# Kernel optimization log

Measured on AMD Instinct MI355X. Metric: run time of the kernel, lower is better.

Reference implementation:

```python
import jax, jax.numpy as jnp
import numpy as np

N = 50000   # nodes
E = 800000  # edges (before self loops)
IN_DIM = 64
HID = 128
HEADS = 4
DH = HID // HEADS  # 32 per-head out_feats
L = 3
EPS = 1e-5
NEG_SLOPE = 0.2


def setup_inputs() -> dict:
    key = jax.random.key(0)
    ks = jax.random.split(key, 10)
    s = 0.1  # weight scale for numerical sanity
    return {
        "node_feats": jax.random.normal(ks[0], (N, IN_DIM), jnp.float32),
        "src": jax.random.randint(ks[1], (E,), 0, N, dtype=jnp.int32),
        "dst": jax.random.randint(ks[2], (E,), 0, N, dtype=jnp.int32),
        "W_in": jax.random.normal(ks[3], (IN_DIM, HID), jnp.float32) * s,
        "b_in": jnp.zeros((HID,), jnp.float32),
        "W_src": jax.random.normal(ks[4], (L, HID, HID), jnp.float32) * s,
        "b_src": jnp.zeros((L, HID), jnp.float32),
        "W_dst": jax.random.normal(ks[5], (L, HID, HID), jnp.float32) * s,
        "b_dst": jnp.zeros((L, HID), jnp.float32),
        "attn": jax.random.normal(ks[6], (L, HEADS, DH), jnp.float32) * s,
        "ln_g": jnp.ones((L, HID), jnp.float32),
        "ln_b": jnp.zeros((L, HID), jnp.float32),
    }


def _layer_norm(x, g, b):
    mu = jnp.mean(x, axis=-1, keepdims=True)
    var = jnp.mean((x - mu) ** 2, axis=-1, keepdims=True)
    return (x - mu) * jax.lax.rsqrt(var + EPS) * g + b


def _gatv2(h, s_idx, d_idx, Ws, bs, Wd, bd, a):
    # h: [N, HID]; edges s_idx -> d_idx (self loops included)
    fs = (h @ Ws + bs).reshape(N, HEADS, DH)  # W_src h, source features
    fd = (h @ Wd + bd).reshape(N, HEADS, DH)  # W_dst h, dest features
    e = jax.nn.leaky_relu(fs[s_idx] + fd[d_idx], NEG_SLOPE)   # [E', H, D]
    logits = jnp.einsum('ehd,hd->eh', e, a)                   # [E', H]
    # segment softmax over incoming edges of each destination node
    m = jax.ops.segment_max(logits, d_idx, num_segments=N)    # [N, H]
    p = jnp.exp(logits - m[d_idx])
    z = jax.ops.segment_sum(p, d_idx, num_segments=N)         # [N, H]
    alpha = p / z[d_idx]                                      # [E', H]
    msg = fs[s_idx] * alpha[..., None]                        # [E', H, D]
    out = jax.ops.segment_sum(msg, d_idx, num_segments=N)     # [N, H, D]
    out = out + h.reshape(N, HEADS, DH)  # residual (Identity res_fc)
    return out.reshape(N, HID)


def reference(node_feats, src, dst, W_in, b_in, W_src, b_src, W_dst, b_dst, attn, ln_g, ln_b):
    loop = jnp.arange(N, dtype=src.dtype)
    s_idx = jnp.concatenate([src, loop])  # add_self_loop
    d_idx = jnp.concatenate([dst, loop])
    h = node_feats @ W_in + b_in
    for l in range(L):
        h_new = _gatv2(h, s_idx, d_idx, W_src[l], b_src[l], W_dst[l], b_dst[l], attn[l])
        h = _layer_norm(h + h_new, ln_g[l], ln_b[l])
        h = jax.nn.relu(h)
    graph_emb = jnp.mean(h, axis=0, keepdims=True)  # dgl.mean_nodes, batch of 1 graph
    return graph_emb, h
```

## Files before the change

kernel.cpp:

```cpp
#include <hip/hip_runtime.h>
#include <hip/hip_bf16.h>

#define NN 50000
#define CSTRIDE 16

typedef short short8 __attribute__((ext_vector_type(8)));
typedef float f32x4 __attribute__((ext_vector_type(4)));

#define GLOBAL_AS __attribute__((address_space(1)))
#define LDS_AS __attribute__((address_space(3)))

__device__ __forceinline__ unsigned short f2bf(float f) {
    unsigned int b = __float_as_uint(f);
    unsigned int r = (b + 0x7FFFu + ((b >> 16) & 1u)) >> 16;
    return (unsigned short)r;
}
__device__ __forceinline__ float bf2f(unsigned short u) {
    return __uint_as_float((unsigned int)u << 16);
}


__global__ __launch_bounds__(256, 4) void prep_kernel(
        const int* __restrict__ dst, int* countsS, int* __restrict__ rank, int E,
        const float* __restrict__ Ws, const float* __restrict__ Wd,
        unsigned short* __restrict__ WtL,
        const float* __restrict__ x, const float* __restrict__ Win,
        const float* __restrict__ bin, unsigned short* __restrict__ hB) {
    int HB = (E + 255) >> 8;
    int blk = blockIdx.x;
    if (blk < HB) {
        int i = blk * 256 + threadIdx.x;
        if (i < E) rank[i] = atomicAdd(&countsS[(size_t)dst[i] * CSTRIDE], 1);
        return;
    }
    if (blk < HB + 384) {
        int e = (blk - HB) * 256 + threadIdx.x;
        int l = e >> 15;
        int r = e & 32767;
        int colc = r >> 7;
        int k = r & 127;
        float v = (colc < 128) ? Ws[l * 16384 + k * 128 + colc]
                               : Wd[l * 16384 + k * 128 + (colc - 128)];
        WtL[l * 32768 + colc * 128 + k] = f2bf(v);
        return;
    }
    int blk0 = blk - HB - 384;
    int tid = threadIdx.x;
    int w = tid >> 6, l = tid & 63;
    int m = l & 15, q = l >> 4;
    short8 B[2][2];
    #pragma unroll
    for (int ct = 0; ct < 2; ++ct) {
        int colw = w * 32 + ct * 16 + m;
        #pragma unroll
        for (int kt = 0; kt < 2; ++kt) {
            short8 a;
            #pragma unroll
            for (int jj = 0; jj < 8; ++jj)
                a[jj] = (short)f2bf(Win[(kt * 32 + q * 8 + jj) * 128 + colw]);
            B[ct][kt] = a;
        }
    }
    float bias[2];
    #pragma unroll
    for (int ct = 0; ct < 2; ++ct) bias[ct] = bin[w * 32 + ct * 16 + m];
    for (int rg = blk0; rg < NN / 16; rg += 512) {
        int row0 = rg * 16;
        const float* ap = x + (size_t)(row0 + m) * 64 + q * 8;
        short8 A[2];
        #pragma unroll
        for (int kt = 0; kt < 2; ++kt) {
            float4 f0 = *(const float4*)(ap + kt * 32);
            float4 f1 = *(const float4*)(ap + kt * 32 + 4);
            short8 a;
            a[0] = (short)f2bf(f0.x); a[1] = (short)f2bf(f0.y);
            a[2] = (short)f2bf(f0.z); a[3] = (short)f2bf(f0.w);
            a[4] = (short)f2bf(f1.x); a[5] = (short)f2bf(f1.y);
            a[6] = (short)f2bf(f1.z); a[7] = (short)f2bf(f1.w);
            A[kt] = a;
        }
        f32x4 acc[2];
        #pragma unroll
        for (int ct = 0; ct < 2; ++ct) acc[ct] = (f32x4){0.f, 0.f, 0.f, 0.f};
        #pragma unroll
        for (int kt = 0; kt < 2; ++kt)
            #pragma unroll
            for (int ct = 0; ct < 2; ++ct)
                acc[ct] = __builtin_amdgcn_mfma_f32_16x16x32_bf16(A[kt], B[ct][kt], acc[ct], 0, 0, 0);
        #pragma unroll
        for (int ct = 0; ct < 2; ++ct) {
            int colw = w * 32 + ct * 16 + m;
            #pragma unroll
            for (int i = 0; i < 4; ++i) {
                int row = row0 + q * 4 + i;
                hB[(size_t)row * 128 + colw] = f2bf(acc[ct][i] + bias[ct]);
            }
        }
    }
}

__global__ __launch_bounds__(256) void alloc_kernel(const int* __restrict__ countsS,
                                                    int* __restrict__ row_beg,
                                                    int* total, int n) {
    int i = blockIdx.x * blockDim.x + threadIdx.x;
    int lane = threadIdx.x & 63;
    int len = (i < n) ? (countsS[(size_t)i * CSTRIDE] + 1) : 0;
    int p = len;
    #pragma unroll
    for (int off = 1; off < 64; off <<= 1) {
        int t = __shfl_up(p, off);
        if (lane >= off) p += t;
    }
    int tot = __shfl(p, 63);
    int base = 0;
    if (lane == 63) base = atomicAdd(total, tot);
    base = __shfl(base, 63);
    if (i < n) row_beg[i] = base + p - len;
}

__device__ __forceinline__ void dual_body(const unsigned short* __restrict__ hB,
                                          const unsigned short* __restrict__ Wt,
                                          const float* __restrict__ bs,
                                          const float* __restrict__ bd,
                                          unsigned short* __restrict__ fsB,
                                          unsigned short* __restrict__ fdB,
                                          unsigned short* Atile, int t0, int tstride) {
    int tid = threadIdx.x;
    int w = tid >> 6, l = tid & 63;
    int m = l & 15, q = l >> 4;
    short8 B[4][4];
    #pragma unroll
    for (int ct = 0; ct < 4; ++ct) {
        int colw = w * 64 + ct * 16 + m;
        const unsigned short* wp = Wt + colw * 128 + q * 8;
        #pragma unroll
        for (int kt = 0; kt < 4; ++kt) B[ct][kt] = *(const short8*)(wp + kt * 32);
    }
    const float* bptr = (w < 2) ? bs : bd;
    unsigned short* OUT = (w < 2) ? fsB : fdB;
    int ocb = (w * 64) & 127;
    float bias[4];
    #pragma unroll
    for (int ct = 0; ct < 4; ++ct) bias[ct] = bptr[ocb + ct * 16 + m];

    const int NT = (NN + 63) / 64;
    for (int t = t0; t < NT; t += tstride) {
        int row0 = t * 64;
        const char* gsrc = (const char*)(hB + (size_t)row0 * 128);
        #pragma unroll
        for (int c = 0; c < 4; ++c) {
            int off = c * 4096 + tid * 16;
            __builtin_amdgcn_global_load_lds((const GLOBAL_AS void*)(gsrc + off),
                                             (LDS_AS void*)((char*)Atile + off), 16, 0, 0);
        }
        __syncthreads();
        #pragma unroll
        for (int rg = 0; rg < 4; ++rg) {
            const unsigned short* ap = Atile + (rg * 16 + m) * 128 + q * 8;
            short8 A[4];
            #pragma unroll
            for (int kt = 0; kt < 4; ++kt) A[kt] = *(const short8*)(ap + kt * 32);
            f32x4 acc[4];
            #pragma unroll
            for (int ct = 0; ct < 4; ++ct) acc[ct] = (f32x4){0.f, 0.f, 0.f, 0.f};
            #pragma unroll
            for (int kt = 0; kt < 4; ++kt)
                #pragma unroll
                for (int ct = 0; ct < 4; ++ct)
                    acc[ct] = __builtin_amdgcn_mfma_f32_16x16x32_bf16(A[kt], B[ct][kt], acc[ct], 0, 0, 0);
            #pragma unroll
            for (int ct = 0; ct < 4; ++ct) {
                int colw = ocb + ct * 16 + m;
                #pragma unroll
                for (int i = 0; i < 4; ++i) {
                    int row = row0 + rg * 16 + q * 4 + i;
                    if (row < NN) OUT[(size_t)row * 128 + colw] = f2bf(acc[ct][i] + bias[ct]);
                }
            }
        }
        __syncthreads();
    }
}

__global__ __launch_bounds__(256, 4) void scatter_dual_kernel(
        const int* __restrict__ src, const int* __restrict__ dst,
        const int* __restrict__ rank, const int* __restrict__ row_beg,
        const int* __restrict__ countsS, int* __restrict__ col, int E, int n,
        const unsigned short* __restrict__ hB, const unsigned short* __restrict__ Wt,
        const float* __restrict__ bs, const float* __restrict__ bd,
        unsigned short* __restrict__ fsB, unsigned short* __restrict__ fdB) {
    __shared__ unsigned short Atile[64 * 128];
    int SB = (E + n + 255) >> 8;
    if ((int)blockIdx.x < SB) {
        int i = blockIdx.x * 256 + threadIdx.x;
        if (i >= E + n) return;
        if (i < E) {
            col[row_beg[dst[i]] + rank[i]] = src[i];
        } else {
            int v = i - E;
            col[row_beg[v] + countsS[(size_t)v * CSTRIDE]] = v;
        }
        return;
    }
    dual_body(hB, Wt, bs, bd, fsB, fdB, Atile, blockIdx.x - SB, gridDim.x - SB);
}

__global__ __launch_bounds__(256, 4) void dual_gemm_mfma(const unsigned short* __restrict__ hB,
                                                         const unsigned short* __restrict__ Wt,
                                                         const float* __restrict__ bs,
                                                         const float* __restrict__ bd,
                                                         unsigned short* __restrict__ fsB,
                                                         unsigned short* __restrict__ fdB) {
    __shared__ unsigned short Atile[64 * 128];
    dual_body(hB, Wt, bs, bd, fsB, fdB, Atile, blockIdx.x, gridDim.x);
}

__global__ __launch_bounds__(256) void agg_ln_kernel(const unsigned short* __restrict__ h_in,
                                                     const unsigned short* __restrict__ fsB,
                                                     const unsigned short* __restrict__ fdB,
                                                     const int* __restrict__ row_beg,
                                                     const int* __restrict__ countsS,
                                                     const int* __restrict__ col,
                                                     const float* __restrict__ attn,
                                                     const float* __restrict__ ln_g,
                                                     const float* __restrict__ ln_b,
                                                     unsigned short* __restrict__ hb_out,
                                                     float* __restrict__ hf_out, int n) {
    int gwave = (blockIdx.x * blockDim.x + threadIdx.x) >> 6;
    int lane = threadIdx.x & 63;
    int half = lane >> 5;
    int sub = lane & 31;
    int node = gwave * 2 + half;
    if (node >= n) return;
    int f0 = 4 * sub;
    unsigned foff = (unsigned)(f0 * 2);
    const char* fsp = (const char*)fsB;
    ushort4 ud = *(const ushort4*)((const char*)fdB + (((unsigned)node << 8) | foff));
    float4 fd4;
    fd4.x = bf2f(ud.x); fd4.y = bf2f(ud.y); fd4.z = bf2f(ud.z); fd4.w = bf2f(ud.w);
    ushort4 uh = *(const ushort4*)((const char*)h_in + (((unsigned)node << 8) | foff));
    float4 h4;
    h4.x = bf2f(uh.x); h4.y = bf2f(uh.y); h4.z = bf2f(uh.z); h4.w = bf2f(uh.w);
    const float4 a4 = *(const float4*)(attn + f0);
    float4 a06, a04;
    a06.x = 0.6f * a4.x; a06.y = 0.6f * a4.y; a06.z = 0.6f * a4.z; a06.w = 0.6f * a4.w;
    a04.x = 0.4f * a4.x; a04.y = 0.4f * a4.y; a04.z = 0.4f * a4.z; a04.w = 0.4f * a4.w;
    int beg = row_beg[node], end = beg + countsS[(size_t)node * CSTRIDE] + 1;

    float z[4];
    float4 acc[4];
    #pragma unroll
    for (int k = 0; k < 4; ++k) {
        z[k] = 0.f;
        acc[k].x = 0.f; acc[k].y = 0.f; acc[k].z = 0.f; acc[k].w = 0.f;
    }

    int j = beg;
    for (; j + 3 < end; j += 4) {
        int s0 = col[j], s1 = col[j + 1], s2 = col[j + 2], s3 = col[j + 3];
        ushort4 u0 = *(const ushort4*)(fsp + (((unsigned)s0 << 8) | foff));
        ushort4 u1 = *(const ushort4*)(fsp + (((unsigned)s1 << 8) | foff));
        ushort4 u2 = *(const ushort4*)(fsp + (((unsigned)s2 << 8) | foff));
        ushort4 u3 = *(const ushort4*)(fsp + (((unsigned)s3 << 8) | foff));
        float4 v0, v1, v2, v3;
        v0.x = bf2f(u0.x); v0.y = bf2f(u0.y); v0.z = bf2f(u0.z); v0.w = bf2f(u0.w);
        v1.x = bf2f(u1.x); v1.y = bf2f(u1.y); v1.z = bf2f(u1.z); v1.w = bf2f(u1.w);
        v2.x = bf2f(u2.x); v2.y = bf2f(u2.y); v2.z = bf2f(u2.z); v2.w = bf2f(u2.w);
        v3.x = bf2f(u3.x); v3.y = bf2f(u3.y); v3.z = bf2f(u3.z); v3.w = bf2f(u3.w);
        float p0, p1, p2, p3;
        {
            float e0 = v0.x + fd4.x, e1 = v0.y + fd4.y, e2 = v0.z + fd4.z, e3 = v0.w + fd4.w;
            p0 = e0 * a06.x + fabsf(e0) * a04.x + e1 * a06.y + fabsf(e1) * a04.y
               + e2 * a06.z + fabsf(e2) * a04.z + e3 * a06.w + fabsf(e3) * a04.w;
        }
        {
            float e0 = v1.x + fd4.x, e1 = v1.y + fd4.y, e2 = v1.z + fd4.z, e3 = v1.w + fd4.w;
            p1 = e0 * a06.x + fabsf(e0) * a04.x + e1 * a06.y + fabsf(e1) * a04.y
               + e2 * a06.z + fabsf(e2) * a04.z + e3 * a06.w + fabsf(e3) * a04.w;
        }
        {
            float e0 = v2.x + fd4.x, e1 = v2.y + fd4.y, e2 = v2.z + fd4.z, e3 = v2.w + fd4.w;
            p2 = e0 * a06.x + fabsf(e0) * a04.x + e1 * a06.y + fabsf(e1) * a04.y
               + e2 * a06.z + fabsf(e2) * a04.z + e3 * a06.w + fabsf(e3) * a04.w;
        }
        {
            float e0 = v3.x + fd4.x, e1 = v3.y + fd4.y, e2 = v3.z + fd4.z, e3 = v3.w + fd4.w;
            p3 = e0 * a06.x + fabsf(e0) * a04.x + e1 * a06.y + fabsf(e1) * a04.y
               + e2 * a06.z + fabsf(e2) * a04.z + e3 * a06.w + fabsf(e3) * a04.w;
        }
        #pragma unroll
        for (int off = 1; off <= 4; off <<= 1) {
            p0 += __shfl_xor(p0, off);
            p1 += __shfl_xor(p1, off);
            p2 += __shfl_xor(p2, off);
            p3 += __shfl_xor(p3, off);
        }
        float w0 = __expf(p0), w1 = __expf(p1), w2 = __expf(p2), w3 = __expf(p3);
        z[0] += w0; z[1] += w1; z[2] += w2; z[3] += w3;
        acc[0].x += w0 * v0.x; acc[0].y += w0 * v0.y; acc[0].z += w0 * v0.z; acc[0].w += w0 * v0.w;
        acc[1].x += w1 * v1.x; acc[1].y += w1 * v1.y; acc[1].z += w1 * v1.z; acc[1].w += w1 * v1.w;
        acc[2].x += w2 * v2.x; acc[2].y += w2 * v2.y; acc[2].z += w2 * v2.z; acc[2].w += w2 * v2.w;
        acc[3].x += w3 * v3.x; acc[3].y += w3 * v3.y; acc[3].z += w3 * v3.z; acc[3].w += w3 * v3.w;
    }
    for (; j < end; ++j) {
        int s = col[j];
        ushort4 u = *(const ushort4*)(fsp + (((unsigned)s << 8) | foff));
        float4 v;
        v.x = bf2f(u.x); v.y = bf2f(u.y); v.z = bf2f(u.z); v.w = bf2f(u.w);
        float e0 = v.x + fd4.x, e1 = v.y + fd4.y, e2 = v.z + fd4.z, e3 = v.w + fd4.w;
        float p = e0 * a06.x + fabsf(e0) * a04.x + e1 * a06.y + fabsf(e1) * a04.y
                + e2 * a06.z + fabsf(e2) * a04.z + e3 * a06.w + fabsf(e3) * a04.w;
        p += __shfl_xor(p, 1);
        p += __shfl_xor(p, 2);
        p += __shfl_xor(p, 4);
        float w = __expf(p);
        z[0] += w;
        acc[0].x += w * v.x; acc[0].y += w * v.y; acc[0].z += w * v.z; acc[0].w += w * v.w;
    }
    float zT = (z[0] + z[1]) + (z[2] + z[3]);
    float axT = (acc[0].x + acc[1].x) + (acc[2].x + acc[3].x);
    float ayT = (acc[0].y + acc[1].y) + (acc[2].y + acc[3].y);
    float azT = (acc[0].z + acc[1].z) + (acc[2].z + acc[3].z);
    float awT = (acc[0].w + acc[1].w) + (acc[2].w + acc[3].w);
    float inv = 1.0f / zT;
    float x0 = 2.f * h4.x + axT * inv;
    float x1 = 2.f * h4.y + ayT * inv;
    float x2 = 2.f * h4.z + azT * inv;
    float x3 = 2.f * h4.w + awT * inv;
    float s = (x0 + x1) + (x2 + x3);
    #pragma unroll
    for (int off = 1; off <= 16; off <<= 1) s += __shfl_xor(s, off);
    float mean = s * (1.f / 128.f);
    float d0 = x0 - mean, d1 = x1 - mean, d2 = x2 - mean, d3 = x3 - mean;
    float v = (d0 * d0 + d1 * d1) + (d2 * d2 + d3 * d3);
    #pragma unroll
    for (int off = 1; off <= 16; off <<= 1) v += __shfl_xor(v, off);
    float rstd = rsqrtf(v * (1.f / 128.f) + 1e-5f);
    float4 g4 = *(const float4*)(ln_g + f0);
    float4 bb4 = *(const float4*)(ln_b + f0);
    float4 o;
    o.x = fmaxf(d0 * rstd * g4.x + bb4.x, 0.f);
    o.y = fmaxf(d1 * rstd * g4.y + bb4.y, 0.f);
    o.z = fmaxf(d2 * rstd * g4.z + bb4.z, 0.f);
    o.w = fmaxf(d3 * rstd * g4.w + bb4.w, 0.f);
    if (hf_out) {
        *(float4*)((char*)hf_out + (((unsigned)node << 9) | (unsigned)(f0 * 4))) = o;
    } else {
        ushort4 ob;
        ob.x = f2bf(o.x); ob.y = f2bf(o.y); ob.z = f2bf(o.z); ob.w = f2bf(o.w);
        *(ushort4*)((char*)hb_out + (((unsigned)node << 8) | foff)) = ob;
    }
}


__global__ __launch_bounds__(128) void mean1_kernel(const float* __restrict__ h,
                                                    float* __restrict__ partials, int n) {
    int c = threadIdx.x;
    float acc = 0.f;
    for (int r = blockIdx.x; r < n; r += gridDim.x)
        acc += h[(size_t)r * 128 + c];
    partials[blockIdx.x * 128 + c] = acc;
}

__global__ __launch_bounds__(1024) void mean2_kernel(const float* __restrict__ partials,
                                                     float* __restrict__ out, int nb, int n) {
    __shared__ float smem[8][128];
    int c = threadIdx.x & 127;
    int g = threadIdx.x >> 7;
    float acc = 0.f;
    for (int r = g; r < nb; r += 8)
        acc += partials[r * 128 + c];
    smem[g][c] = acc;
    __syncthreads();
    if (threadIdx.x < 128) {
        float s = 0.f;
        #pragma unroll
        for (int k = 0; k < 8; ++k) s += smem[k][c];
        out[c] = s * (1.f / n);
    }
}

extern "C" void kernel_launch(void* const* d_in, const int* in_sizes, int n_in,
                              void* d_out, int out_size, void* d_ws, size_t ws_size,
                              hipStream_t stream) {
    const float* node_feats = (const float*)d_in[0];
    const int* src = (const int*)d_in[1];
    const int* dst = (const int*)d_in[2];
    const float* W_in = (const float*)d_in[3];
    const float* b_in = (const float*)d_in[4];
    const float* W_src = (const float*)d_in[5];
    const float* b_src = (const float*)d_in[6];
    const float* W_dst = (const float*)d_in[7];
    const float* b_dst = (const float*)d_in[8];
    const float* attn = (const float*)d_in[9];
    const float* ln_g = (const float*)d_in[10];
    const float* ln_b = (const float*)d_in[11];
    float* out = (float*)d_out;

    const int N = NN;
    const int E = in_sizes[1];

    unsigned short* fsB = (unsigned short*)d_ws;
    unsigned short* fdB = fsB + (size_t)N * 128;
    unsigned short* hB = fdB + (size_t)N * 128;
    unsigned short* WtL = hB + (size_t)N * 128;
    unsigned short* WtIn = WtL + 3 * 32768;
    int* countsS = (int*)(WtIn + 8192);
    int* total = countsS + (size_t)N * CSTRIDE;
    int* row_beg = total + 1;
    int* rankb = row_beg + N;
    int* colb = rankb + E;
    float* partials = (float*)(colb + (E + N));

    const int NT = (N + 63) / 64;

    hipMemsetAsync(countsS, 0, ((size_t)N * CSTRIDE + 1) * sizeof(int), stream);
    int HB = (E + 255) / 256;
    prep_kernel<<<HB + 384 + 512, 256, 0, stream>>>(dst, countsS, rankb, E,
                                                    W_src, W_dst, WtL,
                                                    node_feats, W_in, b_in, hB);
    alloc_kernel<<<(N + 255) / 256, 256, 0, stream>>>(countsS, row_beg, total, N);

    int SB = (E + N + 255) / 256;
    scatter_dual_kernel<<<SB + NT, 256, 0, stream>>>(src, dst, rankb, row_beg,
                                                     countsS, colb, E, N,
                                                     hB, WtL, b_src, b_dst, fsB, fdB);

    for (int l = 0; l < 3; ++l) {
        int last = (l == 2);
        if (l > 0)
            dual_gemm_mfma<<<NT, 256, 0, stream>>>(hB, WtL + (size_t)l * 32768,
                                                   b_src + l * 128, b_dst + l * 128,
                                                   fsB, fdB);
        agg_ln_kernel<<<(N + 7) / 8, 256, 0, stream>>>(hB, fsB, fdB, row_beg, countsS, colb,
                                                       attn + l * 128, ln_g + l * 128,
                                                       ln_b + l * 128,
                                                       last ? nullptr : hB,
                                                       last ? (out + 128) : nullptr, N);
    }

    mean1_kernel<<<256, 128, 0, stream>>>(out + 128, partials, N);
    mean2_kernel<<<1, 1024, 0, stream>>>(partials, out, 256, N);
}
```

Before: 411.1 us.

## Replace global padded-atomic degree histogram with LDS-partitioned range histograms

Degree counting and rank assignment move from per-edge global atomics on a padded (stride 16) counts array to 64 blocks. Each block owns a range of 782 destination nodes, scans all edges and does atomics in shared memory, then writes dense counts. This removes the large memset and the contended global atomics. In exchange, every block reads the whole dst array (64x redundant reads) using only 64 blocks, which may limit parallelism. The aggregation code is tidied into helper functions without changing its behaviour.

After: 674.9 us. +64.2%, slower.

```diff
diff --git a/kernel.cpp b/kernel.cpp
--- a/kernel.cpp
+++ b/kernel.cpp
@@ -2,7 +2,8 @@
 #include <hip/hip_bf16.h>
 
 #define NN 50000
-#define CSTRIDE 16
+#define NHB 64
+#define HRNG 782
 
 typedef short short8 __attribute__((ext_vector_type(8)));
 typedef float f32x4 __attribute__((ext_vector_type(4)));
@@ -18,36 +19,63 @@
 __device__ __forceinline__ float bf2f(unsigned short u) {
     return __uint_as_float((unsigned int)u << 16);
 }
-
+__device__ __forceinline__ float4 bfu4(ushort4 u) {
+    float4 v;
+    v.x = bf2f(u.x); v.y = bf2f(u.y); v.z = bf2f(u.z); v.w = bf2f(u.w);
+    return v;
+}
+__device__ __forceinline__ float edge_logit(float4 v, float4 fd4, float4 a06, float4 a04) {
+    float e0 = v.x + fd4.x, e1 = v.y + fd4.y, e2 = v.z + fd4.z, e3 = v.w + fd4.w;
+    return e0 * a06.x + fabsf(e0) * a04.x + e1 * a06.y + fabsf(e1) * a04.y
+         + e2 * a06.z + fabsf(e2) * a04.z + e3 * a06.w + fabsf(e3) * a04.w;
+}
 
 __global__ __launch_bounds__(256, 4) void prep_kernel(
-        const int* __restrict__ dst, int* countsS, int* __restrict__ rank, int E,
+        const int* __restrict__ dst, int* __restrict__ counts, int* __restrict__ rank, int E,
         const float* __restrict__ Ws, const float* __restrict__ Wd,
         unsigned short* __restrict__ WtL,
         const float* __restrict__ x, const float* __restrict__ Win,
         const float* __restrict__ bin, unsigned short* __restrict__ hB) {
-    int HB = (E + 255) >> 8;
+    __shared__ int hcnt[HRNG];
     int blk = blockIdx.x;
-    if (blk < HB) {
-        int i = blk * 256 + threadIdx.x;
-        if (i < E) rank[i] = atomicAdd(&countsS[(size_t)dst[i] * CSTRIDE], 1);
+    int tid = threadIdx.x;
+    if (blk < NHB) {
+        int base = blk * HRNG;
+        int cnt = NN - base; if (cnt > HRNG) cnt = HRNG;
+        for (int k = tid; k < cnt; k += 256) hcnt[k] = 0;
+        __syncthreads();
+        int E4 = E & ~3;
+        for (int i0 = tid * 4; i0 + 3 < E; i0 += 1024) {
+            int4 d4 = *(const int4*)(dst + i0);
+            unsigned r;
+            r = (unsigned)(d4.x - base); if (r < (unsigned)cnt) rank[i0]     = atomicAdd(&hcnt[r], 1);
+            r = (unsigned)(d4.y - base); if (r < (unsigned)cnt) rank[i0 + 1] = atomicAdd(&hcnt[r], 1);
+            r = (unsigned)(d4.z - base); if (r < (unsigned)cnt) rank[i0 + 2] = atomicAdd(&hcnt[r], 1);
+            r = (unsigned)(d4.w - base); if (r < (unsigned)cnt) rank[i0 + 3] = atomicAdd(&hcnt[r], 1);
+        }
+        if (tid < (E - E4)) {
+            int i = E4 + tid;
+            unsigned r = (unsigned)(dst[i] - base);
+            if (r < (unsigned)cnt) rank[i] = atomicAdd(&hcnt[r], 1);
+        }
+        __syncthreads();
+        for (int k = tid; k < cnt; k += 256) counts[base + k] = hcnt[k];
         return;
     }
-    if (blk < HB + 384) {
-        int e = (blk - HB) * 256 + threadIdx.x;
-        int l = e >> 15;
+    int w = tid >> 6, l = tid & 63;
+    int m = l & 15, q = l >> 4;
+    if (blk < NHB + 384) {
+        int e = (blk - NHB) * 256 + tid;
+        int ll = e >> 15;
         int r = e & 32767;
         int colc = r >> 7;
         int k = r & 127;
-        float v = (colc < 128) ? Ws[l * 16384 + k * 128 + colc]
-                               : Wd[l * 16384 + k * 128 + (colc - 128)];
-        WtL[l * 32768 + colc * 128 + k] = f2bf(v);
+        float v = (colc < 128) ? Ws[ll * 16384 + k * 128 + colc]
+                               : Wd[ll * 16384 + k * 128 + (colc - 128)];
+        WtL[ll * 32768 + colc * 128 + k] = f2bf(v);
         return;
     }
-    int blk0 = blk - HB - 384;
-    int tid = threadIdx.x;
-    int w = tid >> 6, l = tid & 63;
-    int m = l & 15, q = l >> 4;
+    int blk0 = blk - NHB - 384;
     short8 B[2][2];
     #pragma unroll
     for (int ct = 0; ct < 2; ++ct) {
@@ -99,12 +127,12 @@
     }
 }
 
-__global__ __launch_bounds__(256) void alloc_kernel(const int* __restrict__ countsS,
+__global__ __launch_bounds__(256) void alloc_kernel(const int* __restrict__ counts,
                                                     int* __restrict__ row_beg,
                                                     int* total, int n) {
     int i = blockIdx.x * blockDim.x + threadIdx.x;
     int lane = threadIdx.x & 63;
-    int len = (i < n) ? (countsS[(size_t)i * CSTRIDE] + 1) : 0;
+    int len = (i < n) ? (counts[i] + 1) : 0;
     int p = len;
     #pragma unroll
     for (int off = 1; off < 64; off <<= 1) {
@@ -185,7 +213,7 @@
 __global__ __launch_bounds__(256, 4) void scatter_dual_kernel(
         const int* __restrict__ src, const int* __restrict__ dst,
         const int* __restrict__ rank, const int* __restrict__ row_beg,
-        const int* __restrict__ countsS, int* __restrict__ col, int E, int n,
+        const int* __restrict__ counts, int* __restrict__ col, int E, int n,
         const unsigned short* __restrict__ hB, const unsigned short* __restrict__ Wt,
         const float* __restrict__ bs, const float* __restrict__ bd,
         unsigned short* __restrict__ fsB, unsigned short* __restrict__ fdB) {
@@ -198,7 +226,7 @@
             col[row_beg[dst[i]] + rank[i]] = src[i];
         } else {
             int v = i - E;
-            col[row_beg[v] + countsS[(size_t)v * CSTRIDE]] = v;
+            col[row_beg[v] + counts[v]] = v;
         }
         return;
     }
@@ -219,7 +247,7 @@
                                                      const unsigned short* __restrict__ fsB,
                                                      const unsigned short* __restrict__ fdB,
                                                      const int* __restrict__ row_beg,
-                                                     const int* __restrict__ countsS,
+                                                     const int* __restrict__ counts,
                                                      const int* __restrict__ col,
                                                      const float* __restrict__ attn,
                                                      const float* __restrict__ ln_g,
@@ -235,17 +263,13 @@
     int f0 = 4 * sub;
     unsigned foff = (unsigned)(f0 * 2);
     const char* fsp = (const char*)fsB;
-    ushort4 ud = *(const ushort4*)((const char*)fdB + (((unsigned)node << 8) | foff));
-    float4 fd4;
-    fd4.x = bf2f(ud.x); fd4.y = bf2f(ud.y); fd4.z = bf2f(ud.z); fd4.w = bf2f(ud.w);
-    ushort4 uh = *(const ushort4*)((const char*)h_in + (((unsigned)node << 8) | foff));
-    float4 h4;
-    h4.x = bf2f(uh.x); h4.y = bf2f(uh.y); h4.z = bf2f(uh.z); h4.w = bf2f(uh.w);
+    float4 fd4 = bfu4(*(const ushort4*)((const char*)fdB + (((unsigned)node << 8) | foff)));
+    float4 h4 = bfu4(*(const ushort4*)((const char*)h_in + (((unsigned)node << 8) | foff)));
     const float4 a4 = *(const float4*)(attn + f0);
     float4 a06, a04;
     a06.x = 0.6f * a4.x; a06.y = 0.6f * a4.y; a06.z = 0.6f * a4.z; a06.w = 0.6f * a4.w;
     a04.x = 0.4f * a4.x; a04.y = 0.4f * a4.y; a04.z = 0.4f * a4.z; a04.w = 0.4f * a4.w;
-    int beg = row_beg[node], end = beg + countsS[(size_t)node * CSTRIDE] + 1;
+    int beg = row_beg[node], end = beg + counts[node] + 1;
 
     float z[4];
     float4 acc[4];
@@ -262,38 +286,15 @@
         ushort4 u1 = *(const ushort4*)(fsp + (((unsigned)s1 << 8) | foff));
         ushort4 u2 = *(const ushort4*)(fsp + (((unsigned)s2 << 8) | foff));
         ushort4 u3 = *(const ushort4*)(fsp + (((unsigned)s3 << 8) | foff));
-        float4 v0, v1, v2, v3;
-        v0.x = bf2f(u0.x); v0.y = bf2f(u0.y); v0.z = bf2f(u0.z); v0.w = bf2f(u0.w);
-        v1.x = bf2f(u1.x); v1.y = bf2f(u1.y); v1.z = bf2f(u1.z); v1.w = bf2f(u1.w);
-        v2.x = bf2f(u2.x); v2.y = bf2f(u2.y); v2.z = bf2f(u2.z); v2.w = bf2f(u2.w);
-        v3.x = bf2f(u3.x); v3.y = bf2f(u3.y); v3.z = bf2f(u3.z); v3.w = bf2f(u3.w);
-        float p0, p1, p2, p3;
-        {
-            float e0 = v0.x + fd4.x, e1 = v0.y + fd4.y, e2 = v0.z + fd4.z, e3 = v0.w + fd4.w;
-            p0 = e0 * a06.x + fabsf(e0) * a04.x + e1 * a06.y + fabsf(e1) * a04.y
-               + e2 * a06.z + fabsf(e2) * a04.z + e3 * a06.w + fabsf(e3) * a04.w;
-        }
-        {
-            float e0 = v1.x + fd4.x, e1 = v1.y + fd4.y, e2 = v1.z + fd4.z, e3 = v1.w + fd4.w;
-            p1 = e0 * a06.x + fabsf(e0) * a04.x + e1 * a06.y + fabsf(e1) * a04.y
-               + e2 * a06.z + fabsf(e2) * a04.z + e3 * a06.w + fabsf(e3) * a04.w;
-        }
-        {
-            float e0 = v2.x + fd4.x, e1 = v2.y + fd4.y, e2 = v2.z + fd4.z, e3 = v2.w + fd4.w;
-            p2 = e0 * a06.x + fabsf(e0) * a04.x + e1 * a06.y + fabsf(e1) * a04.y
-               + e2 * a06.z + fabsf(e2) * a04.z + e3 * a06.w + fabsf(e3) * a04.w;
-        }
-        {
-            float e0 = v3.x + fd4.x, e1 = v3.y + fd4.y, e2 = v3.z + fd4.z, e3 = v3.w + fd4.w;
-            p3 = e0 * a06.x + fabsf(e0) * a04.x + e1 * a06.y + fabsf(e1) * a04.y
-               + e2 * a06.z + fabsf(e2) * a04.z + e3 * a06.w + fabsf(e3) * a04.w;
-        }
+        float4 v0 = bfu4(u0), v1 = bfu4(u1), v2 = bfu4(u2), v3 = bfu4(u3);
+        float p0 = edge_logit(v0, fd4, a06, a04);
+        float p1 = edge_logit(v1, fd4, a06, a04);
+        float p2 = edge_logit(v2, fd4, a06, a04);
+        float p3 = edge_logit(v3, fd4, a06, a04);
         #pragma unroll
         for (int off = 1; off <= 4; off <<= 1) {
-            p0 += __shfl_xor(p0, off);
-            p1 += __shfl_xor(p1, off);
-            p2 += __shfl_xor(p2, off);
-            p3 += __shfl_xor(p3, off);
+            p0 += __shfl_xor(p0, off); p1 += __shfl_xor(p1, off);
+            p2 += __shfl_xor(p2, off); p3 += __shfl_xor(p3, off);
         }
         float w0 = __expf(p0), w1 = __expf(p1), w2 = __expf(p2), w3 = __expf(p3);
         z[0] += w0; z[1] += w1; z[2] += w2; z[3] += w3;
@@ -305,11 +306,8 @@
     for (; j < end; ++j) {
         int s = col[j];
         ushort4 u = *(const ushort4*)(fsp + (((unsigned)s << 8) | foff));
-        float4 v;
-        v.x = bf2f(u.x); v.y = bf2f(u.y); v.z = bf2f(u.z); v.w = bf2f(u.w);
-        float e0 = v.x + fd4.x, e1 = v.y + fd4.y, e2 = v.z + fd4.z, e3 = v.w + fd4.w;
-        float p = e0 * a06.x + fabsf(e0) * a04.x + e1 * a06.y + fabsf(e1) * a04.y
-                + e2 * a06.z + fabsf(e2) * a04.z + e3 * a06.w + fabsf(e3) * a04.w;
+        float4 v = bfu4(u);
+        float p = edge_logit(v, fd4, a06, a04);
         p += __shfl_xor(p, 1);
         p += __shfl_xor(p, 2);
         p += __shfl_xor(p, 4);
@@ -405,8 +403,8 @@
     unsigned short* hB = fdB + (size_t)N * 128;
     unsigned short* WtL = hB + (size_t)N * 128;
     unsigned short* WtIn = WtL + 3 * 32768;
-    int* countsS = (int*)(WtIn + 8192);
-    int* total = countsS + (size_t)N * CSTRIDE;
+    int* counts = (int*)(WtIn + 8192);
+    int* total = counts + N;
     int* row_beg = total + 1;
     int* rankb = row_beg + N;
     int* colb = rankb + E;
@@ -414,16 +412,16 @@
 
     const int NT = (N + 63) / 64;
 
-    hipMemsetAsync(countsS, 0, ((size_t)N * CSTRIDE + 1) * sizeof(int), stream);
-    int HB = (E + 255) / 256;
-    prep_kernel<<<HB + 384 + 512, 256, 0, stream>>>(dst, countsS, rankb, E,
-                                                    W_src, W_dst, WtL,
-                                                    node_feats, W_in, b_in, hB);
-    alloc_kernel<<<(N + 255) / 256, 256, 0, stream>>>(countsS, row_beg, total, N);
+    hipMemsetAsync(total, 0, sizeof(int), stream);
+
+    prep_kernel<<<NHB + 384 + 512, 256, 0, stream>>>(dst, counts, rankb, E,
+                                                     W_src, W_dst, WtL,
+                                                     node_feats, W_in, b_in, hB);
+    alloc_kernel<<<(N + 255) / 256, 256, 0, stream>>>(counts, row_beg, total, N);
 
     int SB = (E + N + 255) / 256;
     scatter_dual_kernel<<<SB + NT, 256, 0, stream>>>(src, dst, rankb, row_beg,
-                                                     countsS, colb, E, N,
+                                                     counts, colb, E, N,
                                                      hB, WtL, b_src, b_dst, fsB, fdB);
 
     for (int l = 0; l < 3; ++l) {
@@ -432,7 +430,7 @@
             dual_gemm_mfma<<<NT, 256, 0, stream>>>(hB, WtL + (size_t)l * 32768,
                                                    b_src + l * 128, b_dst + l * 128,
                                                    fsB, fdB);
-        agg_ln_kernel<<<(N + 7) / 8, 256, 0, stream>>>(hB, fsB, fdB, row_beg, countsS, colb,
+        agg_ln_kernel<<<(N + 7) / 8, 256, 0, stream>>>(hB, fsB, fdB, row_beg, counts, colb,
                                                        attn + l * 128, ln_g + l * 128,
                                                        ln_b + l * 128,
                                                        last ? nullptr : hB,
```
